# Kernel tuning notes

Measured on AMD Instinct MI355X. Metric: run time of the kernel, lower is better.

The kernel has to match this reference:

```python
import jax, jax.numpy as jnp
import numpy as np

# Model dims
E, K, D, F = 8, 2, 1024, 2048   # num_experts, top_k, d_model, d_ff
B, S = 2, 1024                  # batch, seq -> T = 2048 tokens


def setup_inputs() -> dict:
    key = jax.random.key(0)
    k1, k2, k3, k4 = jax.random.split(key, 4)
    hidden = jax.random.normal(k1, (B, S, D), dtype=jnp.float32)
    gate_logits = jax.random.normal(k2, (B * S, E), dtype=jnp.float32)
    # Expert FFN params: expert_e(x) = silu(x @ W1[e]) @ W2[e]
    W1 = jax.random.normal(k3, (E, D, F), dtype=jnp.float32) * 0.02
    W2 = jax.random.normal(k4, (E, F, D), dtype=jnp.float32) * 0.02
    return {"hidden": hidden, "gate_logits": gate_logits, "W1": W1, "W2": W2}


def reference(hidden, gate_logits, W1, W2):
    b, s, d = hidden.shape
    x = hidden.reshape(-1, d)                                  # [T, D]
    # Router: softmax -> top-k -> renormalize (gate_logits path of forward)
    probs = jax.nn.softmax(gate_logits, axis=-1)               # [T, E]
    topk_w, topk_idx = jax.lax.top_k(probs, K)                 # [T, K]
    topk_w = topk_w / jnp.sum(topk_w, axis=-1, keepdims=True)
    # Combine weights as a dense [T, E] map (top_k indices are distinct)
    tok_w = jnp.sum(jax.nn.one_hot(topk_idx, E, dtype=topk_w.dtype)
                    * topk_w[..., None], axis=1)               # [T, E]
    # Grouped expert FFN, expressed densely over the expert axis; the
    # combine weights zero out non-selected experts, so the math equals the
    # original gather -> per-expert GEMM -> weighted scatter-combine.
    h = jax.nn.silu(jnp.einsum('td,edf->tef', x, W1))          # [T, E, F]
    y = jnp.einsum('tef,efd->ted', h, W2)                      # [T, E, D]
    out = jnp.einsum('te,ted->td', tok_w, y)                   # [T, D]
    return out.reshape(b, s, d)
```

## Files before the change

kernel.cpp:

```cpp
#include <hip/hip_runtime.h>
#include <hip/hip_bf16.h>

#define E_N 8
#define D_DIM 1024
#define F_DIM 2048
#define T_N 2048
#define NSLOT 4096

typedef unsigned short u16;
typedef unsigned int u32;
typedef float floatx4 __attribute__((ext_vector_type(4)));
typedef short bf16x8v __attribute__((ext_vector_type(8)));

__device__ __forceinline__ u16 f2bf(float f) {
    union { float f; u32 u; } v; v.f = f;
    u32 r = v.u + 0x7FFFu + ((v.u >> 16) & 1u);
    return (u16)(r >> 16);
}

__device__ __forceinline__ void gll16(const void* g, void* l) {
    __builtin_amdgcn_global_load_lds((const __attribute__((address_space(1))) void*)g,
                                     (__attribute__((address_space(3))) void*)l, 16, 0, 0);
}

__global__ void router_kernel(const float* __restrict__ gl,
                              int* __restrict__ cnt, int* __restrict__ base,
                              int* __restrict__ slot_tok, int* __restrict__ tok_slot,
                              float* __restrict__ tok_w) {
    __shared__ int scnt[E_N];
    __shared__ int sbase[E_N];
    const int tid = threadIdx.x;
    if (tid < E_N) scnt[tid] = 0;
    __syncthreads();
    int e0a[8], e1a[8], p0a[8], p1a[8];
    float w0a[8];
#pragma unroll
    for (int i = 0; i < 8; ++i) {
        const int t = tid + i * 256;
        const float4* gp = (const float4*)(gl + (size_t)t * E_N);
        const float4 x0 = gp[0], x1 = gp[1];
        float l[E_N] = {x0.x, x0.y, x0.z, x0.w, x1.x, x1.y, x1.z, x1.w};
        int e0 = 0; float m0 = l[0];
#pragma unroll
        for (int e = 1; e < E_N; ++e) if (l[e] > m0) { m0 = l[e]; e0 = e; }
        int e1 = -1; float m1 = -1e30f;
#pragma unroll
        for (int e = 0; e < E_N; ++e) if (e != e0 && l[e] > m1) { m1 = l[e]; e1 = e; }
        const float p = __expf(m1 - m0);
        w0a[i] = 1.0f / (1.0f + p);
        e0a[i] = e0; e1a[i] = e1;
        p0a[i] = atomicAdd(&scnt[e0], 1);
        p1a[i] = atomicAdd(&scnt[e1], 1);
    }
    __syncthreads();
    if (tid == 0) {
        int s = 0;
        for (int e = 0; e < E_N; ++e) { sbase[e] = s; base[e] = s; cnt[e] = scnt[e]; s += scnt[e]; }
    }
    __syncthreads();
#pragma unroll
    for (int i = 0; i < 8; ++i) {
        const int t = tid + i * 256;
        const int s0 = sbase[e0a[i]] + p0a[i];
        const int s1 = sbase[e1a[i]] + p1a[i];
        slot_tok[s0] = t; slot_tok[s1] = t;
        tok_slot[2 * t] = s0; tok_slot[2 * t + 1] = s1;
        tok_w[2 * t] = w0a[i]; tok_w[2 * t + 1] = 1.0f - w0a[i];
    }
}

__global__ __launch_bounds__(256) void gather_x_kernel(const float* __restrict__ X,
                                                       const int* __restrict__ slot_tok,
                                                       u16* __restrict__ Xg) {
    const int s = blockIdx.x, t = threadIdx.x;
    const int tok = slot_tok[s];
    const float4 v = *(const float4*)(X + (size_t)tok * D_DIM + t * 4);
    union { u16 o[4]; uint2 q; } u;
    u.o[0] = f2bf(v.x); u.o[1] = f2bf(v.y); u.o[2] = f2bf(v.z); u.o[3] = f2bf(v.w);
    *(uint2*)(Xg + (size_t)s * D_DIM + t * 4) = u.q;
}

__global__ __launch_bounds__(256) void cvt_t_kernel(const float* __restrict__ src,
                                                    u16* __restrict__ dst, int R, int C) {
    const int e = blockIdx.z;
    const int r0 = blockIdx.y << 6, c0 = blockIdx.x << 6;
    __shared__ __align__(16) u16 LT[4096];
    const int t = threadIdx.x;
    const int rowb = t >> 4;
    const int col4 = t & 15;
    const float* sp = src + (size_t)e * R * C + (size_t)(r0 + rowb) * C + c0 + col4 * 4;
#pragma unroll
    for (int rr = 0; rr < 4; ++rr) {
        const float4 v = *(const float4*)(sp + (size_t)(rr * 16) * C);
        const int r = rowb + rr * 16;
        const int rg = r >> 3, ro = r & 7;
        u16 b[4] = {f2bf(v.x), f2bf(v.y), f2bf(v.z), f2bf(v.w)};
#pragma unroll
        for (int j = 0; j < 4; ++j) {
            const int c = col4 * 4 + j;
            LT[c * 64 + ((rg ^ ((c >> 2) & 7)) << 3) + ro] = b[j];
        }
    }
    __syncthreads();
    u16* dp = dst + (size_t)e * R * C;
#pragma unroll
    for (int i = 0; i < 2; ++i) {
        const int id = i * 256 + t;
        const int c = id >> 3, seg = id & 7;
        const uint4 q = *(const uint4*)&LT[c * 64 + ((seg ^ ((c >> 2) & 7)) << 3)];
        *(uint4*)(dp + (size_t)(c0 + c) * R + r0 + seg * 8) = q;
    }
}

template<bool G1>
__global__ __launch_bounds__(256) void moe_gemm_kernel(
        const u16* __restrict__ A, const u16* __restrict__ B,
        const int* __restrict__ cnt, const int* __restrict__ basep,
        u16* __restrict__ hout, float* __restrict__ yout) {
    constexpr int KA = G1 ? D_DIM : F_DIM;
    constexpr int KB = KA;
    constexpr int KIT = 16;
    const int e  = G1 ? blockIdx.z : (blockIdx.z >> 1);
    const int kh = G1 ? 0 : (blockIdx.z & 1);
    const int mt = blockIdx.y;
    const int nt = blockIdx.x;
    const int cnt_e = cnt[e];
    if (mt * 128 >= cnt_e) return;
    const int m0 = basep[e] + mt * 128;
    const int vm = cnt_e - mt * 128;

    __shared__ __align__(16) u16 Alds[8192];
    __shared__ __align__(16) u16 Blds[8192];

    const int tid = threadIdx.x;
    const int wid = tid >> 6, lane = tid & 63;
    const int l3 = lane >> 3, l7 = lane & 7;
    const int stgRow = wid * 8 + l3;
    const int stgCol = ((l7 ^ l3) << 3);

    const u16* aS = A + (size_t)(m0 + stgRow) * KA + kh * (F_DIM / 2) + stgCol;
    const u16* bS = B + (size_t)e * ((size_t)D_DIM * F_DIM)
                      + (size_t)(nt * 128 + stgRow) * KB + kh * (F_DIM / 2) + stgCol;

    const int wm = (wid >> 1) * 64, wn = (wid & 1) * 64;
    const int lr = lane & 15, lq = lane >> 4;
    const int aoff = (wm + lr) * 64;
    const int boff = (wn + lr) * 64;
    const int sw0 = ((lq)     ^ l7) << 3;
    const int sw1 = ((lq + 4) ^ l7) << 3;

    floatx4 acc[4][4];
    const floatx4 zero = {0.f, 0.f, 0.f, 0.f};
#pragma unroll
    for (int i = 0; i < 4; ++i)
#pragma unroll
        for (int j = 0; j < 4; ++j) acc[i][j] = zero;

    for (int kt = 0; kt < KIT; ++kt) {
#pragma unroll
        for (int c = 0; c < 4; ++c) {
            gll16(aS + (size_t)(c * 32) * KA, &Alds[c * 2048 + wid * 512]);
            gll16(bS + (size_t)(c * 32) * KB, &Blds[c * 2048 + wid * 512]);
        }
        aS += 64; bS += 64;
        __syncthreads();
#pragma unroll
        for (int ks = 0; ks < 2; ++ks) {
            const int sw = ks ? sw1 : sw0;
            bf16x8v af[4], bfv[4];
#pragma unroll
            for (int mi = 0; mi < 4; ++mi) af[mi]  = *(const bf16x8v*)&Alds[aoff + mi * 1024 + sw];
#pragma unroll
            for (int ni = 0; ni < 4; ++ni) bfv[ni] = *(const bf16x8v*)&Blds[boff + ni * 1024 + sw];
#pragma unroll
            for (int mi = 0; mi < 4; ++mi)
#pragma unroll
                for (int ni = 0; ni < 4; ++ni)
                    acc[mi][ni] = __builtin_amdgcn_mfma_f32_16x16x32_bf16(af[mi], bfv[ni], acc[mi][ni], 0, 0, 0);
        }
        __syncthreads();
    }

    if constexpr (G1) {
#pragma unroll
        for (int mi = 0; mi < 4; ++mi)
#pragma unroll
            for (int r = 0; r < 4; ++r) {
                const int rl = wm + mi * 16 + lq * 4 + r;
                if (rl < vm) {
                    u16* hp = hout + (size_t)(m0 + rl) * F_DIM + nt * 128 + wn + lr;
#pragma unroll
                    for (int ni = 0; ni < 4; ++ni) {
                        const float v = acc[mi][ni][r];
                        hp[ni * 16] = f2bf(v / (1.0f + __expf(-v)));
                    }
                }
            }
    } else {
        float* Y = yout + (size_t)kh * NSLOT * D_DIM;
#pragma unroll
        for (int mi = 0; mi < 4; ++mi)
#pragma unroll
            for (int r = 0; r < 4; ++r) {
                const int rl = wm + mi * 16 + lq * 4 + r;
                if (rl < vm) {
                    float* yp = Y + (size_t)(m0 + rl) * D_DIM + nt * 128 + wn + lr;
#pragma unroll
                    for (int ni = 0; ni < 4; ++ni) yp[ni * 16] = acc[mi][ni][r];
                }
            }
    }
}

__global__ __launch_bounds__(256) void combine_kernel(const float* __restrict__ Y,
                                                      const int* __restrict__ tok_slot,
                                                      const float* __restrict__ tok_w,
                                                      float* __restrict__ out) {
    const int t = blockIdx.x, tid = threadIdx.x;
    const int s0 = tok_slot[2 * t], s1 = tok_slot[2 * t + 1];
    const float w0 = tok_w[2 * t], w1 = tok_w[2 * t + 1];
    const float* y0 = Y;
    const float* y1 = Y + (size_t)NSLOT * D_DIM;
    const float4 a0 = *(const float4*)(y0 + (size_t)s0 * D_DIM + tid * 4);
    const float4 a1 = *(const float4*)(y1 + (size_t)s0 * D_DIM + tid * 4);
    const float4 b0 = *(const float4*)(y0 + (size_t)s1 * D_DIM + tid * 4);
    const float4 b1 = *(const float4*)(y1 + (size_t)s1 * D_DIM + tid * 4);
    float4 o;
    o.x = w0 * (a0.x + a1.x) + w1 * (b0.x + b1.x);
    o.y = w0 * (a0.y + a1.y) + w1 * (b0.y + b1.y);
    o.z = w0 * (a0.z + a1.z) + w1 * (b0.z + b1.z);
    o.w = w0 * (a0.w + a1.w) + w1 * (b0.w + b1.w);
    *(float4*)(out + (size_t)t * D_DIM + tid * 4) = o;
}

extern "C" void kernel_launch(void* const* d_in, const int* in_sizes, int n_in,
                              void* d_out, int out_size, void* d_ws, size_t ws_size,
                              hipStream_t stream) {
    const float* hidden = (const float*)d_in[0];
    const float* gl     = (const float*)d_in[1];
    const float* W1     = (const float*)d_in[2];
    const float* W2     = (const float*)d_in[3];
    float* out = (float*)d_out;

    char* ws = (char*)d_ws;
    int* m = (int*)ws;
    int* cnt      = m;
    int* basep    = m + 16;
    int* slot_tok = m + 32;
    int* tok_slot = m + 32 + 4096;
    float* tok_w  = (float*)(m + 32 + 8192);

    const size_t YBYTES = (size_t)2 * NSLOT * D_DIM * 4;
    const size_t HBYTES = (size_t)(NSLOT + 128) * F_DIM * 2;
    float* Y = (float*)(ws + (1 << 16));
    u16* h   = (u16*)(ws + (1 << 16) + YBYTES);
    char* regionR = ws + (1 << 16) + YBYTES + HBYTES;
    u16* W1T = (u16*)regionR;
    u16* Xg  = (u16*)(regionR + (size_t)E_N * D_DIM * F_DIM * 2);
    u16* W2T = (u16*)regionR;

    router_kernel<<<1, 256, 0, stream>>>(gl, cnt, basep, slot_tok, tok_slot, tok_w);
    gather_x_kernel<<<NSLOT, 256, 0, stream>>>(hidden, slot_tok, Xg);
    cvt_t_kernel<<<dim3(F_DIM / 64, D_DIM / 64, E_N), 256, 0, stream>>>(W1, W1T, D_DIM, F_DIM);
    moe_gemm_kernel<true><<<dim3(F_DIM / 128, 16, E_N), 256, 0, stream>>>(Xg, W1T, cnt, basep, h, nullptr);
    cvt_t_kernel<<<dim3(D_DIM / 64, F_DIM / 64, E_N), 256, 0, stream>>>(W2, W2T, F_DIM, D_DIM);
    moe_gemm_kernel<false><<<dim3(D_DIM / 128, 16, E_N * 2), 256, 0, stream>>>(h, W2T, cnt, basep, nullptr, Y);
    combine_kernel<<<T_N, 256, 0, stream>>>(Y, tok_slot, tok_w, out);
}
```

Baseline: 256.5 us.

## Fuse prep kernels, double-buffer GEMM LDS, fold combine into atomic epilogue

Merges the gather and both weight-transpose conversions into one prep kernel with a revised LDS swizzle and packed 64-bit writes. Adds double-buffered LDS staging in the grouped GEMM so the next K tile loads while the current one is computed, removing one barrier per iteration. Applies the routing weight in the first GEMM's SiLU epilogue and has the second GEMM atomically add straight into the output, which drops the fp32 Y buffer and the combine kernel. The cost is a memset of the output, float atomic contention from two K-halves and two experts per token, and nondeterministic summation order.

Result: slower. 297.7 us (+16.1%).

```diff
diff --git a/kernel.cpp b/kernel.cpp
--- a/kernel.cpp
+++ b/kernel.cpp
@@ -9,6 +9,7 @@
 
 typedef unsigned short u16;
 typedef unsigned int u32;
+typedef unsigned long long u64;
 typedef float floatx4 __attribute__((ext_vector_type(4)));
 typedef short bf16x8v __attribute__((ext_vector_type(8)));
 
@@ -25,8 +26,7 @@
 
 __global__ void router_kernel(const float* __restrict__ gl,
                               int* __restrict__ cnt, int* __restrict__ base,
-                              int* __restrict__ slot_tok, int* __restrict__ tok_slot,
-                              float* __restrict__ tok_w) {
+                              int* __restrict__ slot_tok, float* __restrict__ slot_w) {
     __shared__ int scnt[E_N];
     __shared__ int sbase[E_N];
     const int tid = threadIdx.x;
@@ -64,42 +64,26 @@
         const int s0 = sbase[e0a[i]] + p0a[i];
         const int s1 = sbase[e1a[i]] + p1a[i];
         slot_tok[s0] = t; slot_tok[s1] = t;
-        tok_slot[2 * t] = s0; tok_slot[2 * t + 1] = s1;
-        tok_w[2 * t] = w0a[i]; tok_w[2 * t + 1] = 1.0f - w0a[i];
-    }
-}
-
-__global__ __launch_bounds__(256) void gather_x_kernel(const float* __restrict__ X,
-                                                       const int* __restrict__ slot_tok,
-                                                       u16* __restrict__ Xg) {
-    const int s = blockIdx.x, t = threadIdx.x;
-    const int tok = slot_tok[s];
-    const float4 v = *(const float4*)(X + (size_t)tok * D_DIM + t * 4);
-    union { u16 o[4]; uint2 q; } u;
-    u.o[0] = f2bf(v.x); u.o[1] = f2bf(v.y); u.o[2] = f2bf(v.z); u.o[3] = f2bf(v.w);
-    *(uint2*)(Xg + (size_t)s * D_DIM + t * 4) = u.q;
-}
-
-__global__ __launch_bounds__(256) void cvt_t_kernel(const float* __restrict__ src,
-                                                    u16* __restrict__ dst, int R, int C) {
-    const int e = blockIdx.z;
-    const int r0 = blockIdx.y << 6, c0 = blockIdx.x << 6;
-    __shared__ __align__(16) u16 LT[4096];
+        slot_w[s0] = w0a[i]; slot_w[s1] = 1.0f - w0a[i];
+    }
+}
+
+__device__ __forceinline__ void cvt_tile(const float* __restrict__ src, u16* __restrict__ dst,
+                                         int R, int C, int tr, int tc, int e, char* LT) {
+    const int r0 = tr << 6, c0 = tc << 6;
     const int t = threadIdx.x;
-    const int rowb = t >> 4;
-    const int col4 = t & 15;
-    const float* sp = src + (size_t)e * R * C + (size_t)(r0 + rowb) * C + c0 + col4 * 4;
-#pragma unroll
-    for (int rr = 0; rr < 4; ++rr) {
-        const float4 v = *(const float4*)(sp + (size_t)(rr * 16) * C);
-        const int r = rowb + rr * 16;
-        const int rg = r >> 3, ro = r & 7;
-        u16 b[4] = {f2bf(v.x), f2bf(v.y), f2bf(v.z), f2bf(v.w)};
-#pragma unroll
-        for (int j = 0; j < 4; ++j) {
-            const int c = col4 * 4 + j;
-            LT[c * 64 + ((rg ^ ((c >> 2) & 7)) << 3) + ro] = b[j];
-        }
+    const int rowq = t >> 4, col4 = t & 15;
+    const float* sp = src + (size_t)e * R * C + (size_t)(r0 + rowq * 4) * C + c0 + col4 * 4;
+    float4 v[4];
+#pragma unroll
+    for (int i = 0; i < 4; ++i) v[i] = *(const float4*)(sp + (size_t)i * C);
+    const float* f = (const float*)v;
+#pragma unroll
+    for (int j = 0; j < 4; ++j) {
+        const int c = col4 * 4 + j;
+        u64 pk = (u64)f2bf(f[0 * 4 + j]) | ((u64)f2bf(f[1 * 4 + j]) << 16)
+               | ((u64)f2bf(f[2 * 4 + j]) << 32) | ((u64)f2bf(f[3 * 4 + j]) << 48);
+        *(u64*)(LT + c * 144 + ((rowq ^ col4) << 3)) = pk;
     }
     __syncthreads();
     u16* dp = dst + (size_t)e * R * C;
@@ -107,8 +91,42 @@
     for (int i = 0; i < 2; ++i) {
         const int id = i * 256 + t;
         const int c = id >> 3, seg = id & 7;
-        const uint4 q = *(const uint4*)&LT[c * 64 + ((seg ^ ((c >> 2) & 7)) << 3)];
-        *(uint4*)(dp + (size_t)(c0 + c) * R + r0 + seg * 8) = q;
+        const int x = (c >> 2) & 15;
+        const u64 lo = *(const u64*)(LT + c * 144 + (((2 * seg) ^ x) << 3));
+        const u64 hi = *(const u64*)(LT + c * 144 + (((2 * seg + 1) ^ x) << 3));
+        u64 q[2] = {lo, hi};
+        *(uint4*)(dp + (size_t)(c0 + c) * R + r0 + seg * 8) = *(const uint4*)q;
+    }
+}
+
+__global__ __launch_bounds__(256) void prep_kernel(const float* __restrict__ W1,
+                                                   const float* __restrict__ W2,
+                                                   const float* __restrict__ X,
+                                                   const int* __restrict__ slot_tok,
+                                                   u16* __restrict__ W1T, u16* __restrict__ W2T,
+                                                   u16* __restrict__ Xg) {
+    __shared__ __align__(16) char LT[64 * 144];
+    const int b = blockIdx.x;
+    if (b < 4096) {
+        const int e = b >> 9, rem = b & 511;
+        cvt_tile(W1, W1T, D_DIM, F_DIM, rem >> 5, rem & 31, e, LT);
+    } else if (b < 8192) {
+        const int e = (b - 4096) >> 9, rem = (b - 4096) & 511;
+        cvt_tile(W2, W2T, F_DIM, D_DIM, rem >> 4, rem & 15, e, LT);
+    } else {
+        const int g = b - 8192;
+        const int t = threadIdx.x;
+        const int s = 4 * g + (t >> 6), lane = t & 63;
+        const int tok = slot_tok[s];
+        const float* xp = X + (size_t)tok * D_DIM + lane * 4;
+        u16* gp = Xg + (size_t)s * D_DIM + lane * 4;
+#pragma unroll
+        for (int p = 0; p < 4; ++p) {
+            const float4 v = *(const float4*)(xp + p * 256);
+            union { u16 o[4]; uint2 q; } u;
+            u.o[0] = f2bf(v.x); u.o[1] = f2bf(v.y); u.o[2] = f2bf(v.z); u.o[3] = f2bf(v.w);
+            *(uint2*)(gp + p * 256) = u.q;
+        }
     }
 }
 
@@ -116,7 +134,8 @@
 __global__ __launch_bounds__(256) void moe_gemm_kernel(
         const u16* __restrict__ A, const u16* __restrict__ B,
         const int* __restrict__ cnt, const int* __restrict__ basep,
-        u16* __restrict__ hout, float* __restrict__ yout) {
+        const int* __restrict__ slot_tok, const float* __restrict__ slot_w,
+        u16* __restrict__ hout, float* __restrict__ out) {
     constexpr int KA = G1 ? D_DIM : F_DIM;
     constexpr int KB = KA;
     constexpr int KIT = 16;
@@ -129,8 +148,8 @@
     const int m0 = basep[e] + mt * 128;
     const int vm = cnt_e - mt * 128;
 
-    __shared__ __align__(16) u16 Alds[8192];
-    __shared__ __align__(16) u16 Blds[8192];
+    __shared__ __align__(16) u16 Alds[2][8192];
+    __shared__ __align__(16) u16 Blds[2][8192];
 
     const int tid = threadIdx.x;
     const int wid = tid >> 6, lane = tid & 63;
@@ -156,29 +175,35 @@
 #pragma unroll
         for (int j = 0; j < 4; ++j) acc[i][j] = zero;
 
+    auto stage = [&](int buf, int kt) {
+        const int ko = kt * 64;
+#pragma unroll
+        for (int c = 0; c < 4; ++c) {
+            gll16(aS + ko + (size_t)(c * 32) * KA, &Alds[buf][c * 2048 + wid * 512]);
+            gll16(bS + ko + (size_t)(c * 32) * KB, &Blds[buf][c * 2048 + wid * 512]);
+        }
+    };
+
+    stage(0, 0);
+    int cur = 0;
     for (int kt = 0; kt < KIT; ++kt) {
-#pragma unroll
-        for (int c = 0; c < 4; ++c) {
-            gll16(aS + (size_t)(c * 32) * KA, &Alds[c * 2048 + wid * 512]);
-            gll16(bS + (size_t)(c * 32) * KB, &Blds[c * 2048 + wid * 512]);
-        }
-        aS += 64; bS += 64;
         __syncthreads();
+        if (kt + 1 < KIT) stage(cur ^ 1, kt + 1);
 #pragma unroll
         for (int ks = 0; ks < 2; ++ks) {
             const int sw = ks ? sw1 : sw0;
             bf16x8v af[4], bfv[4];
 #pragma unroll
-            for (int mi = 0; mi < 4; ++mi) af[mi]  = *(const bf16x8v*)&Alds[aoff + mi * 1024 + sw];
-#pragma unroll
-            for (int ni = 0; ni < 4; ++ni) bfv[ni] = *(const bf16x8v*)&Blds[boff + ni * 1024 + sw];
+            for (int mi = 0; mi < 4; ++mi) af[mi]  = *(const bf16x8v*)&Alds[cur][aoff + mi * 1024 + sw];
+#pragma unroll
+            for (int ni = 0; ni < 4; ++ni) bfv[ni] = *(const bf16x8v*)&Blds[cur][boff + ni * 1024 + sw];
 #pragma unroll
             for (int mi = 0; mi < 4; ++mi)
 #pragma unroll
                 for (int ni = 0; ni < 4; ++ni)
                     acc[mi][ni] = __builtin_amdgcn_mfma_f32_16x16x32_bf16(af[mi], bfv[ni], acc[mi][ni], 0, 0, 0);
         }
-        __syncthreads();
+        cur ^= 1;
     }
 
     if constexpr (G1) {
@@ -188,49 +213,29 @@
             for (int r = 0; r < 4; ++r) {
                 const int rl = wm + mi * 16 + lq * 4 + r;
                 if (rl < vm) {
+                    const float w = slot_w[m0 + rl];
                     u16* hp = hout + (size_t)(m0 + rl) * F_DIM + nt * 128 + wn + lr;
 #pragma unroll
                     for (int ni = 0; ni < 4; ++ni) {
                         const float v = acc[mi][ni][r];
-                        hp[ni * 16] = f2bf(v / (1.0f + __expf(-v)));
+                        hp[ni * 16] = f2bf(w * v / (1.0f + __expf(-v)));
                     }
                 }
             }
     } else {
-        float* Y = yout + (size_t)kh * NSLOT * D_DIM;
 #pragma unroll
         for (int mi = 0; mi < 4; ++mi)
 #pragma unroll
             for (int r = 0; r < 4; ++r) {
                 const int rl = wm + mi * 16 + lq * 4 + r;
                 if (rl < vm) {
-                    float* yp = Y + (size_t)(m0 + rl) * D_DIM + nt * 128 + wn + lr;
-#pragma unroll
-                    for (int ni = 0; ni < 4; ++ni) yp[ni * 16] = acc[mi][ni][r];
+                    const int tok = slot_tok[m0 + rl];
+                    float* op = out + (size_t)tok * D_DIM + nt * 128 + wn + lr;
+#pragma unroll
+                    for (int ni = 0; ni < 4; ++ni) atomicAdd(&op[ni * 16], acc[mi][ni][r]);
                 }
             }
     }
-}
-
-__global__ __launch_bounds__(256) void combine_kernel(const float* __restrict__ Y,
-                                                      const int* __restrict__ tok_slot,
-                                                      const float* __restrict__ tok_w,
-                                                      float* __restrict__ out) {
-    const int t = blockIdx.x, tid = threadIdx.x;
-    const int s0 = tok_slot[2 * t], s1 = tok_slot[2 * t + 1];
-    const float w0 = tok_w[2 * t], w1 = tok_w[2 * t + 1];
-    const float* y0 = Y;
-    const float* y1 = Y + (size_t)NSLOT * D_DIM;
-    const float4 a0 = *(const float4*)(y0 + (size_t)s0 * D_DIM + tid * 4);
-    const float4 a1 = *(const float4*)(y1 + (size_t)s0 * D_DIM + tid * 4);
-    const float4 b0 = *(const float4*)(y0 + (size_t)s1 * D_DIM + tid * 4);
-    const float4 b1 = *(const float4*)(y1 + (size_t)s1 * D_DIM + tid * 4);
-    float4 o;
-    o.x = w0 * (a0.x + a1.x) + w1 * (b0.x + b1.x);
-    o.y = w0 * (a0.y + a1.y) + w1 * (b0.y + b1.y);
-    o.z = w0 * (a0.z + a1.z) + w1 * (b0.z + b1.z);
-    o.w = w0 * (a0.w + a1.w) + w1 * (b0.w + b1.w);
-    *(float4*)(out + (size_t)t * D_DIM + tid * 4) = o;
 }
 
 extern "C" void kernel_launch(void* const* d_in, const int* in_sizes, int n_in,
@@ -247,23 +252,21 @@
     int* cnt      = m;
     int* basep    = m + 16;
     int* slot_tok = m + 32;
-    int* tok_slot = m + 32 + 4096;
-    float* tok_w  = (float*)(m + 32 + 8192);
-
-    const size_t YBYTES = (size_t)2 * NSLOT * D_DIM * 4;
-    const size_t HBYTES = (size_t)(NSLOT + 128) * F_DIM * 2;
-    float* Y = (float*)(ws + (1 << 16));
-    u16* h   = (u16*)(ws + (1 << 16) + YBYTES);
-    char* regionR = ws + (1 << 16) + YBYTES + HBYTES;
-    u16* W1T = (u16*)regionR;
-    u16* Xg  = (u16*)(regionR + (size_t)E_N * D_DIM * F_DIM * 2);
-    u16* W2T = (u16*)regionR;
-
-    router_kernel<<<1, 256, 0, stream>>>(gl, cnt, basep, slot_tok, tok_slot, tok_w);
-    gather_x_kernel<<<NSLOT, 256, 0, stream>>>(hidden, slot_tok, Xg);
-    cvt_t_kernel<<<dim3(F_DIM / 64, D_DIM / 64, E_N), 256, 0, stream>>>(W1, W1T, D_DIM, F_DIM);
-    moe_gemm_kernel<true><<<dim3(F_DIM / 128, 16, E_N), 256, 0, stream>>>(Xg, W1T, cnt, basep, h, nullptr);
-    cvt_t_kernel<<<dim3(D_DIM / 64, F_DIM / 64, E_N), 256, 0, stream>>>(W2, W2T, F_DIM, D_DIM);
-    moe_gemm_kernel<false><<<dim3(D_DIM / 128, 16, E_N * 2), 256, 0, stream>>>(h, W2T, cnt, basep, nullptr, Y);
-    combine_kernel<<<T_N, 256, 0, stream>>>(Y, tok_slot, tok_w, out);
-}
+    float* slot_w = (float*)(m + 32 + 4096);
+
+    const size_t HBYTES  = (size_t)(NSLOT + 128) * F_DIM * 2;
+    const size_t W1BYTES = (size_t)E_N * D_DIM * F_DIM * 2;
+    const size_t XBYTES  = (size_t)(NSLOT + 128) * D_DIM * 2;
+    u16* h   = (u16*)(ws + (1 << 16));
+    u16* W1T = (u16*)(ws + (1 << 16) + HBYTES);
+    u16* Xg  = (u16*)(ws + (1 << 16) + HBYTES + W1BYTES);
+    u16* W2T = (u16*)(ws + (1 << 16) + HBYTES + W1BYTES + XBYTES);
+
+    hipMemsetAsync(d_out, 0, (size_t)out_size * sizeof(float), stream);
+    router_kernel<<<1, 256, 0, stream>>>(gl, cnt, basep, slot_tok, slot_w);
+    prep_kernel<<<8192 + NSLOT / 4, 256, 0, stream>>>(W1, W2, hidden, slot_tok, W1T, W2T, Xg);
+    moe_gemm_kernel<true><<<dim3(F_DIM / 128, 16, E_N), 256, 0, stream>>>(
+        Xg, W1T, cnt, basep, slot_tok, slot_w, h, nullptr);
+    moe_gemm_kernel<false><<<dim3(D_DIM / 128, 16, E_N * 2), 256, 0, stream>>>(
+        h, W2T, cnt, basep, slot_tok, slot_w, nullptr, out);
+}
```
